# Kernel tuning notes

Measured on AMD Instinct MI355X. Metric: run time of the kernel, lower is better.

The kernel has to match this reference:

```python
import jax, jax.numpy as jnp
import numpy as np

B, N, F, FNEW = 2, 16384, 16, 16

def setup_inputs() -> dict:
    key = jax.random.key(0)
    k1, k2, k3, k4 = jax.random.split(key, 4)
    scale = 0.02
    x = jax.random.normal(k1, (B, N, F), dtype=jnp.float32)
    A = jax.random.normal(k2, (N, N), dtype=jnp.float32)
    kernel = jax.random.normal(k3, (N, F, FNEW), dtype=jnp.float32) * scale
    bias = jax.random.normal(k4, (N, FNEW), dtype=jnp.float32) * scale
    return {"x": x, "A": A, "kernel": kernel, "bias": bias}

def reference(x, A, kernel, bias):
    # Per-node batched matmul: original tiles x to [B,N,F,FNEW], multiplies by
    # kernel [N,F,FNEW] and reduce_sums over F. Equivalent fused einsum:
    h = jnp.einsum('bnf,nfg->bng', x, kernel)        # [B, N, FNEW]
    # Dense adjacency aggregation: tf.matmul(A, h) broadcast over batch.
    out = jnp.einsum('nm,bmg->bng', A, h)            # [B, N, FNEW]
    return out + bias                                # bias [N, FNEW] broadcasts
```

## Files before the change

### kernel.cpp

```cpp
#include <hip/hip_runtime.h>
#include <hip/hip_bf16.h>

#define NN 16384

typedef __attribute__((ext_vector_type(4))) float  f32x4;
typedef __attribute__((ext_vector_type(8))) short  s16x8;
typedef __attribute__((ext_vector_type(4))) short  s16x4;

__device__ inline short bf16_of(float f) {
    return __builtin_bit_cast(short, __float2bfloat16(f));
}

__global__ void fuse_h(const float* __restrict__ x, const float* __restrict__ ker,
                       __hip_bfloat16* __restrict__ hpt) {
    int tid = blockIdx.x * 256 + threadIdx.x;
    int g = tid & 15;
    int m = tid >> 4;
    const float* xb0 = x + m * 16;
    const float* xb1 = x + NN * 16 + m * 16;
    const float* kp  = ker + m * 256 + g;
    float h0 = 0.f, h1 = 0.f;
#pragma unroll
    for (int f = 0; f < 16; ++f) {
        float kk = kp[f * 16];
        h0 += xb0[f] * kk;
        h1 += xb1[f] * kk;
    }
    hpt[g * NN + m]        = __float2bfloat16(h0);
    hpt[(16 + g) * NN + m] = __float2bfloat16(h1);
}

__global__ __launch_bounds__(256, 4) void gcn_partial(
        const float* __restrict__ A,
        const __hip_bfloat16* __restrict__ hpt,
        float* __restrict__ part) {
    __shared__ __attribute__((aligned(16))) char tile[4][8192];

    const int lane = threadIdx.x & 63;
    const int wave = threadIdx.x >> 6;
    const int rowBlk = blockIdx.x >> 2;
    const int ks     = blockIdx.x & 3;
    const int n0     = rowBlk * 64 + wave * 16;
    const int kbase  = ks * 4096;

    const int row  = lane & 15;
    const int kg   = lane >> 4;

    char* lds = tile[wave];

    f32x4 acc0 = {0.f, 0.f, 0.f, 0.f};
    f32x4 acc1 = {0.f, 0.f, 0.f, 0.f};
    f32x4 st[16];

    const float* abase = A + (size_t)n0 * NN + kbase;
    const __hip_bfloat16* b0base = hpt + row * NN + kbase + kg * 8;
    const __hip_bfloat16* b1base = b0base + 16 * NN;

#pragma unroll
    for (int r = 0; r < 16; ++r)
        st[r] = __builtin_nontemporal_load(
                    (const f32x4*)(abase + (size_t)r * NN + lane * 4));
#pragma unroll
    for (int r = 0; r < 16; ++r) {
        int byte = (r * 512 + lane * 8) ^ ((r & 7) << 4);
        s16x4 v;
        v[0] = bf16_of(st[r][0]); v[1] = bf16_of(st[r][1]);
        v[2] = bf16_of(st[r][2]); v[3] = bf16_of(st[r][3]);
        *(s16x4*)(lds + byte) = v;
    }

#pragma unroll 1
    for (int t = 0; t < 16; ++t) {
        s16x8 bb0[4], bb1[4];
#pragma unroll
        for (int j = 0; j < 4; ++j) {
            bb0[j] = *(const s16x8*)(b0base + t * 256 + j * 32);
            bb1[j] = *(const s16x8*)(b1base + t * 256 + j * 32);
        }
        if (t < 15) {
            const float* ap = abase + (t + 1) * 256 + lane * 4;
#pragma unroll
            for (int r = 0; r < 16; ++r)
                st[r] = __builtin_nontemporal_load(
                            (const f32x4*)(ap + (size_t)r * NN));
        }
#pragma unroll
        for (int j = 0; j < 4; ++j) {
            int byte = (row * 512 + j * 64 + kg * 16) ^ ((row & 7) << 4);
            s16x8 af = *(const s16x8*)(lds + byte);
            acc0 = __builtin_amdgcn_mfma_f32_16x16x32_bf16(af, bb0[j], acc0, 0, 0, 0);
            acc1 = __builtin_amdgcn_mfma_f32_16x16x32_bf16(af, bb1[j], acc1, 0, 0, 0);
        }
        s16x8 cb0[4], cb1[4];
#pragma unroll
        for (int j = 0; j < 4; ++j) {
            cb0[j] = *(const s16x8*)(b0base + t * 256 + 128 + j * 32);
            cb1[j] = *(const s16x8*)(b1base + t * 256 + 128 + j * 32);
        }
#pragma unroll
        for (int j = 0; j < 4; ++j) {
            int byte = (row * 512 + 256 + j * 64 + kg * 16) ^ ((row & 7) << 4);
            s16x8 af = *(const s16x8*)(lds + byte);
            acc0 = __builtin_amdgcn_mfma_f32_16x16x32_bf16(af, cb0[j], acc0, 0, 0, 0);
            acc1 = __builtin_amdgcn_mfma_f32_16x16x32_bf16(af, cb1[j], acc1, 0, 0, 0);
        }
        if (t < 15) {
#pragma unroll
            for (int r = 0; r < 16; ++r) {
                int byte = (r * 512 + lane * 8) ^ ((r & 7) << 4);
                s16x4 v;
                v[0] = bf16_of(st[r][0]); v[1] = bf16_of(st[r][1]);
                v[2] = bf16_of(st[r][2]); v[3] = bf16_of(st[r][3]);
                *(s16x4*)(lds + byte) = v;
            }
        }
    }

    float* pb = part + (size_t)ks * (NN * 32);
#pragma unroll
    for (int i = 0; i < 4; ++i) {
        int n = n0 + kg * 4 + i;
        pb[n * 32 + row]      = acc0[i];
        pb[n * 32 + 16 + row] = acc1[i];
    }
}

__global__ void gcn_reduce(const float* __restrict__ part,
                           const float* __restrict__ bias,
                           float* __restrict__ out) {
    int idx = blockIdx.x * 256 + threadIdx.x;
    int n = idx >> 5, c = idx & 31;
    int b = c >> 4, g = c & 15;
    float s = part[idx] + part[idx + NN * 32] + part[idx + 2 * NN * 32]
            + part[idx + 3 * NN * 32];
    out[(size_t)b * (NN * 16) + n * 16 + g] = s + bias[n * 16 + g];
}

extern "C" void kernel_launch(void* const* d_in, const int* in_sizes, int n_in,
                              void* d_out, int out_size, void* d_ws, size_t ws_size,
                              hipStream_t stream) {
    const float* x    = (const float*)d_in[0];
    const float* A    = (const float*)d_in[1];
    const float* ker  = (const float*)d_in[2];
    const float* bias = (const float*)d_in[3];
    float* out = (float*)d_out;
    __hip_bfloat16* hpt = (__hip_bfloat16*)d_ws;
    float* part = (float*)((char*)d_ws + (1 << 20));

    fuse_h<<<dim3(NN * 16 / 256), dim3(256), 0, stream>>>(x, ker, hpt);
    gcn_partial<<<dim3(1024), dim3(256), 0, stream>>>(A, hpt, part);
    gcn_reduce<<<dim3(NN * 32 / 256), dim3(256), 0, stream>>>(part, bias, out);
}
```

Baseline: 222.7 us.

## Drop split-K: one wave per 16-row block with staggered K start, fused bias

```diff
diff --git a/kernel.cpp b/kernel.cpp
--- a/kernel.cpp
+++ b/kernel.cpp
@@ -30,36 +30,31 @@
     hpt[(16 + g) * NN + m] = __float2bfloat16(h1);
 }
 
-__global__ __launch_bounds__(256, 4) void gcn_partial(
+__global__ __launch_bounds__(64, 1) void gcn_main(
         const float* __restrict__ A,
         const __hip_bfloat16* __restrict__ hpt,
-        float* __restrict__ part) {
-    __shared__ __attribute__((aligned(16))) char tile[4][8192];
+        const float* __restrict__ bias,
+        float* __restrict__ out) {
+    __shared__ __attribute__((aligned(16))) char lds[8192];
 
-    const int lane = threadIdx.x & 63;
-    const int wave = threadIdx.x >> 6;
-    const int rowBlk = blockIdx.x >> 2;
-    const int ks     = blockIdx.x & 3;
-    const int n0     = rowBlk * 64 + wave * 16;
-    const int kbase  = ks * 4096;
-
+    const int lane = threadIdx.x;
+    const int n0   = blockIdx.x * 16;
     const int row  = lane & 15;
     const int kg   = lane >> 4;
-
-    char* lds = tile[wave];
+    const int phase = blockIdx.x & 63;
 
     f32x4 acc0 = {0.f, 0.f, 0.f, 0.f};
     f32x4 acc1 = {0.f, 0.f, 0.f, 0.f};
     f32x4 st[16];
 
-    const float* abase = A + (size_t)n0 * NN + kbase;
-    const __hip_bfloat16* b0base = hpt + row * NN + kbase + kg * 8;
+    const float* abase = A + (size_t)n0 * NN;
+    const __hip_bfloat16* b0base = hpt + row * NN + kg * 8;
     const __hip_bfloat16* b1base = b0base + 16 * NN;
 
 #pragma unroll
     for (int r = 0; r < 16; ++r)
         st[r] = __builtin_nontemporal_load(
-                    (const f32x4*)(abase + (size_t)r * NN + lane * 4));
+                    (const f32x4*)(abase + (size_t)r * NN + phase * 256 + lane * 4));
 #pragma unroll
     for (int r = 0; r < 16; ++r) {
         int byte = (r * 512 + lane * 8) ^ ((r & 7) << 4);
@@ -70,15 +65,17 @@
     }
 
 #pragma unroll 1
-    for (int t = 0; t < 16; ++t) {
+    for (int t = 0; t < 64; ++t) {
+        const int s  = (phase + t) & 63;
+        const int sn = (phase + t + 1) & 63;
         s16x8 bb0[4], bb1[4];
 #pragma unroll
         for (int j = 0; j < 4; ++j) {
-            bb0[j] = *(const s16x8*)(b0base + t * 256 + j * 32);
-            bb1[j] = *(const s16x8*)(b1base + t * 256 + j * 32);
+            bb0[j] = *(const s16x8*)(b0base + s * 256 + j * 32);
+            bb1[j] = *(const s16x8*)(b1base + s * 256 + j * 32);
         }
-        if (t < 15) {
-            const float* ap = abase + (t + 1) * 256 + lane * 4;
+        if (t < 63) {
+            const float* ap = abase + sn * 256 + lane * 4;
 #pragma unroll
             for (int r = 0; r < 16; ++r)
                 st[r] = __builtin_nontemporal_load(
@@ -94,8 +91,8 @@
         s16x8 cb0[4], cb1[4];
 #pragma unroll
         for (int j = 0; j < 4; ++j) {
-            cb0[j] = *(const s16x8*)(b0base + t * 256 + 128 + j * 32);
-            cb1[j] = *(const s16x8*)(b1base + t * 256 + 128 + j * 32);
+            cb0[j] = *(const s16x8*)(b0base + s * 256 + 128 + j * 32);
+            cb1[j] = *(const s16x8*)(b1base + s * 256 + 128 + j * 32);
         }
 #pragma unroll
         for (int j = 0; j < 4; ++j) {
@@ -104,7 +101,7 @@
             acc0 = __builtin_amdgcn_mfma_f32_16x16x32_bf16(af, cb0[j], acc0, 0, 0, 0);
             acc1 = __builtin_amdgcn_mfma_f32_16x16x32_bf16(af, cb1[j], acc1, 0, 0, 0);
         }
-        if (t < 15) {
+        if (t < 63) {
 #pragma unroll
             for (int r = 0; r < 16; ++r) {
                 int byte = (r * 512 + lane * 8) ^ ((r & 7) << 4);
@@ -116,24 +113,13 @@
         }
     }
 
-    float* pb = part + (size_t)ks * (NN * 32);
 #pragma unroll
     for (int i = 0; i < 4; ++i) {
         int n = n0 + kg * 4 + i;
-        pb[n * 32 + row]      = acc0[i];
-        pb[n * 32 + 16 + row] = acc1[i];
+        float bv = bias[n * 16 + row];
+        out[(size_t)0 * (NN * 16) + n * 16 + row] = acc0[i] + bv;
+        out[(size_t)1 * (NN * 16) + n * 16 + row] = acc1[i] + bv;
     }
-}
-
-__global__ void gcn_reduce(const float* __restrict__ part,
-                           const float* __restrict__ bias,
-                           float* __restrict__ out) {
-    int idx = blockIdx.x * 256 + threadIdx.x;
-    int n = idx >> 5, c = idx & 31;
-    int b = c >> 4, g = c & 15;
-    float s = part[idx] + part[idx + NN * 32] + part[idx + 2 * NN * 32]
-            + part[idx + 3 * NN * 32];
-    out[(size_t)b * (NN * 16) + n * 16 + g] = s + bias[n * 16 + g];
 }
 
 extern "C" void kernel_launch(void* const* d_in, const int* in_sizes, int n_in,
@@ -145,9 +131,7 @@
     const float* bias = (const float*)d_in[3];
     float* out = (float*)d_out;
     __hip_bfloat16* hpt = (__hip_bfloat16*)d_ws;
-    float* part = (float*)((char*)d_ws + (1 << 20));
 
     fuse_h<<<dim3(NN * 16 / 256), dim3(256), 0, stream>>>(x, ker, hpt);
-    gcn_partial<<<dim3(1024), dim3(256), 0, stream>>>(A, hpt, part);
-    gcn_reduce<<<dim3(NN * 32 / 256), dim3(256), 0, stream>>>(part, bias, out);
+    gcn_main<<<dim3(NN / 16), dim3(64), 0, stream>>>(A, hpt, bias, out);
 }
```

Result: no change. 226.3 us (+1.6%).
